# Performance work log

Hardware: AMD Instinct MI355X
Metric: run time of the kernel (lower is better)

## Reference

```python
import jax, jax.numpy as jnp
import numpy as np

MARGIN = 1.0  # init kwarg 'margin'
NUM_CLASSES = 16


def setup_inputs() -> dict:
    key = jax.random.key(0)
    k1, k2 = jax.random.split(key)
    embeddings = jax.random.normal(k1, (384, 1024), dtype=jnp.float32)
    labels = jax.random.randint(k2, (384,), 0, NUM_CLASSES, dtype=jnp.int64)
    return {"embeddings": embeddings, "labels": labels}


def reference(embeddings, labels):
    # Dense, on-device equivalent of the CPU triplet mining:
    # valid triplet (a, p, n) iff labels[a]==labels[p], a<p, labels[n]!=labels[a].
    # Mean over all valid triplets == original torch losses.mean().
    B = embeddings.shape[0]
    sq = jnp.sum(embeddings * embeddings, axis=1)                      # [B]
    # Squared pairwise distances via Gram matrix (same math as (x_i-x_j)^2.sum())
    D = sq[:, None] + sq[None, :] - 2.0 * (embeddings @ embeddings.T)  # [B,B]

    eq = labels[:, None] == labels[None, :]                            # same-label mask [B,B]
    idx = jnp.arange(B)
    ap_valid = eq & (idx[:, None] < idx[None, :])                      # anchor<positive pairs
    mask = ap_valid[:, :, None] & (~eq)[:, None, :]                    # [a,p,n] valid triplets

    # loss[a,p,n] = relu(D[a,p] - D[a,n] + margin)
    loss = jax.nn.relu(D[:, :, None] - D[:, None, :] + MARGIN)         # [B,B,B]

    count = jnp.sum(mask)
    total = jnp.sum(jnp.where(mask, loss, jnp.float32(0.0)))
    mean = jnp.where(count > 0, total / count.astype(loss.dtype), jnp.float32(0.0))
    return mean, count
```

## Files before the change

kernel.cpp:

```cpp
#include <hip/hip_runtime.h>


constexpr int BN  = 384;
constexpr int DIM = 1024;
constexpr float MARGIN = 1.0f;
constexpr int LDK = 68;

__global__ __launch_bounds__(256) void gram_kernel(
    const float* __restrict__ E, float* __restrict__ P,
    float* __restrict__ sqpart, float* __restrict__ total,
    int* __restrict__ cnt, int* __restrict__ ticket, int KC, int NZ) {
    __shared__ float Ast[32 * LDK];
    __shared__ float Bst[32 * LDK];
    const int t    = threadIdx.x;
    const int tile = blockIdx.x % 36;
    const int z    = blockIdx.x / 36;
    const int ti   = tile / 6, tj = tile % 6;
    const int i0   = ti * 64, j0 = tj * 64;

    if (blockIdx.x == 0 && t == 0) { *total = 0.f; *cnt = 0; *ticket = 0; }

    const int r  = t >> 2;
    const int kq = t & 3;
    const int kb = kq * 8;
    const int rs = r ^ (kq << 4);

    const float* Ab = E + (size_t)(i0 + r) * DIM + z * KC + kb;
    const float* Bb = E + (size_t)(j0 + r) * DIM + z * KC + kb;

    float4 a0 = *(const float4*)(Ab);
    float4 a1 = *(const float4*)(Ab + 4);
    float4 b0 = *(const float4*)(Bb);
    float4 b1 = *(const float4*)(Bb + 4);

    const int tx = t & 15, ty = t >> 4;
    float acc[4][4] = {};

    for (int kt = 0; kt < KC; kt += 32) {
        Ast[(kb + 0) * LDK + rs] = a0.x; Ast[(kb + 1) * LDK + rs] = a0.y;
        Ast[(kb + 2) * LDK + rs] = a0.z; Ast[(kb + 3) * LDK + rs] = a0.w;
        Ast[(kb + 4) * LDK + rs] = a1.x; Ast[(kb + 5) * LDK + rs] = a1.y;
        Ast[(kb + 6) * LDK + rs] = a1.z; Ast[(kb + 7) * LDK + rs] = a1.w;
        Bst[(kb + 0) * LDK + rs] = b0.x; Bst[(kb + 1) * LDK + rs] = b0.y;
        Bst[(kb + 2) * LDK + rs] = b0.z; Bst[(kb + 3) * LDK + rs] = b0.w;
        Bst[(kb + 4) * LDK + rs] = b1.x; Bst[(kb + 5) * LDK + rs] = b1.y;
        Bst[(kb + 6) * LDK + rs] = b1.z; Bst[(kb + 7) * LDK + rs] = b1.w;
        __syncthreads();
        if (kt + 32 < KC) {
            a0 = *(const float4*)(Ab + kt + 32);
            a1 = *(const float4*)(Ab + kt + 36);
            b0 = *(const float4*)(Bb + kt + 32);
            b1 = *(const float4*)(Bb + kt + 36);
        }
#pragma unroll
        for (int kk = 0; kk < 32; ++kk) {
            const int sw = (kk >> 3) << 4;
            const float4 av = *(const float4*)&Ast[kk * LDK + ((4 * ty) ^ sw)];
            const float4 bv = *(const float4*)&Bst[kk * LDK + ((4 * tx) ^ sw)];
            const float aa[4] = {av.x, av.y, av.z, av.w};
            const float bb[4] = {bv.x, bv.y, bv.z, bv.w};
#pragma unroll
            for (int i2 = 0; i2 < 4; ++i2)
#pragma unroll
                for (int j2 = 0; j2 < 4; ++j2)
                    acc[i2][j2] += aa[i2] * bb[j2];
        }
        __syncthreads();
    }

    const size_t rowstride = (size_t)NZ * BN;
#pragma unroll
    for (int i2 = 0; i2 < 4; ++i2) {
        *(float4*)&P[(size_t)(i0 + 4 * ty + i2) * rowstride + (size_t)z * BN + (j0 + 4 * tx)] =
            make_float4(acc[i2][0], acc[i2][1], acc[i2][2], acc[i2][3]);
    }
    if (ti == tj && tx == ty) {
#pragma unroll
        for (int i2 = 0; i2 < 4; ++i2)
            sqpart[z * BN + (i0 + 4 * ty + i2)] = acc[i2][i2];
    }
}

template <int NZ>
__global__ __launch_bounds__(128) void triplet_kernel(
    const float* __restrict__ P, const float* __restrict__ sqpart,
    const int* __restrict__ labels, float* __restrict__ total,
    int* __restrict__ cnt, int* __restrict__ ticket, float* __restrict__ out) {
    __shared__ float Hrow[BN];
    __shared__ int   lab[BN];
    __shared__ int   poslist[BN];
    __shared__ int   npos_s;
    __shared__ float wsum[2];
    __shared__ int   wcnt[2];
    const int a   = blockIdx.x;
    const int tid = threadIdx.x;

    if (tid == 0) npos_s = 0;
    for (int i = tid; i < BN; i += 128) lab[i] = labels[i];

    if (tid < 96) {
        const int c0 = tid * 4;
        float4 g = make_float4(0.f, 0.f, 0.f, 0.f);
        float4 s = make_float4(0.f, 0.f, 0.f, 0.f);
#pragma unroll
        for (int z = 0; z < NZ; ++z) {
            const float4 pv = *(const float4*)&P[(size_t)a * ((size_t)NZ * BN) + z * BN + c0];
            const float4 sv = *(const float4*)&sqpart[z * BN + c0];
            g.x += pv.x; g.y += pv.y; g.z += pv.z; g.w += pv.w;
            s.x += sv.x; s.y += sv.y; s.z += sv.z; s.w += sv.w;
        }
        Hrow[c0 + 0] = s.x - 2.f * g.x;
        Hrow[c0 + 1] = s.y - 2.f * g.y;
        Hrow[c0 + 2] = s.z - 2.f * g.z;
        Hrow[c0 + 3] = s.w - 2.f * g.w;
    }
    __syncthreads();

    const int la = lab[a];
    int lc = 0;
#pragma unroll
    for (int q = 0; q < 3; ++q) {
        const int p = tid + q * 128;
        if (lab[p] != la) ++lc;
        else if (p > a) { const int k = atomicAdd(&npos_s, 1); poslist[k] = p; }
    }
    __syncthreads();
    const int np = npos_s;

    const float hn0 = Hrow[tid];
    const float hn1 = Hrow[tid + 128];
    const float hn2 = Hrow[tid + 256];
    const bool  ng0 = (lab[tid]       != la);
    const bool  ng1 = (lab[tid + 128] != la);
    const bool  ng2 = (lab[tid + 256] != la);

    float ls = 0.f;
    for (int k = 0; k < np; ++k) {
        const float dpm = Hrow[poslist[k]] + MARGIN;
        if (ng0) { const float v = dpm - hn0; ls += (v > 0.f) ? v : 0.f; }
        if (ng1) { const float v = dpm - hn1; ls += (v > 0.f) ? v : 0.f; }
        if (ng2) { const float v = dpm - hn2; ls += (v > 0.f) ? v : 0.f; }
    }

#pragma unroll
    for (int off = 32; off; off >>= 1) {
        ls += __shfl_down(ls, off);
        lc += __shfl_down(lc, off);
    }
    const int wave = tid >> 6, lane = tid & 63;
    if (lane == 0) { wsum[wave] = ls; wcnt[wave] = lc; }
    __syncthreads();
    if (tid == 0) {
        const float s    = wsum[0] + wsum[1];
        const int   nneg = wcnt[0] + wcnt[1];
        if (s != 0.f) atomicAdd(total, s);
        if (np)       atomicAdd(cnt, np * nneg);
        __threadfence();
        const int done = atomicAdd(ticket, 1);
        if (done == (int)gridDim.x - 1) {
            const float tot = atomicAdd(total, 0.0f);
            const int   c   = atomicAdd(cnt, 0);
            out[0] = (c > 0) ? tot / (float)c : 0.f;
            out[1] = (float)c;
        }
    }
}

extern "C" void kernel_launch(void* const* d_in, const int* in_sizes, int n_in,
                              void* d_out, int out_size, void* d_ws, size_t ws_size,
                              hipStream_t stream) {
    const float* E      = (const float*)d_in[0];
    const int*   labels = (const int*)d_in[1];
    float*       out    = (float*)d_out;

    int Z = 1;
    for (int cand : {8, 4, 2}) {
        size_t need = (size_t)cand * BN * BN * 4 + (size_t)cand * BN * 4 + 64;
        if (need <= ws_size) { Z = cand; break; }
    }

    char*  ws     = (char*)d_ws;
    float* P      = (float*)ws;
    float* sqpart = (float*)(ws + (size_t)Z * BN * BN * 4);
    float* total  = (float*)(ws + (size_t)Z * BN * BN * 4 + (size_t)Z * BN * 4);
    int*   cnt    = (int*)(total + 1);
    int*   ticket = (int*)(total + 2);

    gram_kernel<<<36 * Z, 256, 0, stream>>>(E, P, sqpart, total, cnt, ticket, DIM / Z, Z);

    switch (Z) {
        case 8:  triplet_kernel<8><<<BN, 128, 0, stream>>>(P, sqpart, labels, total, cnt, ticket, out); break;
        case 4:  triplet_kernel<4><<<BN, 128, 0, stream>>>(P, sqpart, labels, total, cnt, ticket, out); break;
        case 2:  triplet_kernel<2><<<BN, 128, 0, stream>>>(P, sqpart, labels, total, cnt, ticket, out); break;
        default: triplet_kernel<1><<<BN, 128, 0, stream>>>(P, sqpart, labels, total, cnt, ticket, out); break;
    }
}
```

Measured before the change: 83.06 us.

## Split-K into 16 single-stage chunks and widen triplet kernel to one thread per column

The Gram kernel now always splits K into 16 chunks of 64, loading each chunk into shared memory once with no inner K loop. This puts 576 blocks in flight and removes the loop's barriers. The triplet kernel uses 384 threads, one per column. It counts negatives with a per-label shared histogram and precomputes the positive distances plus margin into shared memory, so the inner loop has no branches. The cost is a larger partial-product workspace with no workspace-size check, and a 16-way reduction per element in the triplet stage.

```diff
diff --git a/kernel.cpp b/kernel.cpp
--- a/kernel.cpp
+++ b/kernel.cpp
@@ -1,17 +1,19 @@
 #include <hip/hip_runtime.h>
 
 
-constexpr int BN  = 384;
-constexpr int DIM = 1024;
+constexpr int   BN     = 384;
+constexpr int   DIM    = 1024;
 constexpr float MARGIN = 1.0f;
-constexpr int LDK = 68;
+constexpr int   Z      = 16;
+constexpr int   KC     = DIM / Z;
+constexpr int   LDK    = 68;
 
 __global__ __launch_bounds__(256) void gram_kernel(
     const float* __restrict__ E, float* __restrict__ P,
     float* __restrict__ sqpart, float* __restrict__ total,
-    int* __restrict__ cnt, int* __restrict__ ticket, int KC, int NZ) {
-    __shared__ float Ast[32 * LDK];
-    __shared__ float Bst[32 * LDK];
+    int* __restrict__ cnt, int* __restrict__ ticket) {
+    __shared__ float Ast[KC * LDK];
+    __shared__ float Bst[KC * LDK];
     const int t    = threadIdx.x;
     const int tile = blockIdx.x % 36;
     const int z    = blockIdx.x / 36;
@@ -22,53 +24,44 @@
 
     const int r  = t >> 2;
     const int kq = t & 3;
-    const int kb = kq * 8;
     const int rs = r ^ (kq << 4);
 
-    const float* Ab = E + (size_t)(i0 + r) * DIM + z * KC + kb;
-    const float* Bb = E + (size_t)(j0 + r) * DIM + z * KC + kb;
+    const float* Ab = E + (size_t)(i0 + r) * DIM + z * KC + kq * 16;
+    const float* Bb = E + (size_t)(j0 + r) * DIM + z * KC + kq * 16;
 
-    float4 a0 = *(const float4*)(Ab);
-    float4 a1 = *(const float4*)(Ab + 4);
-    float4 b0 = *(const float4*)(Bb);
-    float4 b1 = *(const float4*)(Bb + 4);
+    float4 a[4], b[4];
+#pragma unroll
+    for (int q = 0; q < 4; ++q) {
+        a[q] = *(const float4*)(Ab + 4 * q);
+        b[q] = *(const float4*)(Bb + 4 * q);
+    }
+#pragma unroll
+    for (int q = 0; q < 4; ++q) {
+        const int kb = kq * 16 + 4 * q;
+        Ast[(kb + 0) * LDK + rs] = a[q].x; Ast[(kb + 1) * LDK + rs] = a[q].y;
+        Ast[(kb + 2) * LDK + rs] = a[q].z; Ast[(kb + 3) * LDK + rs] = a[q].w;
+        Bst[(kb + 0) * LDK + rs] = b[q].x; Bst[(kb + 1) * LDK + rs] = b[q].y;
+        Bst[(kb + 2) * LDK + rs] = b[q].z; Bst[(kb + 3) * LDK + rs] = b[q].w;
+    }
+    __syncthreads();
 
     const int tx = t & 15, ty = t >> 4;
     float acc[4][4] = {};
-
-    for (int kt = 0; kt < KC; kt += 32) {
-        Ast[(kb + 0) * LDK + rs] = a0.x; Ast[(kb + 1) * LDK + rs] = a0.y;
-        Ast[(kb + 2) * LDK + rs] = a0.z; Ast[(kb + 3) * LDK + rs] = a0.w;
-        Ast[(kb + 4) * LDK + rs] = a1.x; Ast[(kb + 5) * LDK + rs] = a1.y;
-        Ast[(kb + 6) * LDK + rs] = a1.z; Ast[(kb + 7) * LDK + rs] = a1.w;
-        Bst[(kb + 0) * LDK + rs] = b0.x; Bst[(kb + 1) * LDK + rs] = b0.y;
-        Bst[(kb + 2) * LDK + rs] = b0.z; Bst[(kb + 3) * LDK + rs] = b0.w;
-        Bst[(kb + 4) * LDK + rs] = b1.x; Bst[(kb + 5) * LDK + rs] = b1.y;
-        Bst[(kb + 6) * LDK + rs] = b1.z; Bst[(kb + 7) * LDK + rs] = b1.w;
-        __syncthreads();
-        if (kt + 32 < KC) {
-            a0 = *(const float4*)(Ab + kt + 32);
-            a1 = *(const float4*)(Ab + kt + 36);
-            b0 = *(const float4*)(Bb + kt + 32);
-            b1 = *(const float4*)(Bb + kt + 36);
-        }
 #pragma unroll
-        for (int kk = 0; kk < 32; ++kk) {
-            const int sw = (kk >> 3) << 4;
-            const float4 av = *(const float4*)&Ast[kk * LDK + ((4 * ty) ^ sw)];
-            const float4 bv = *(const float4*)&Bst[kk * LDK + ((4 * tx) ^ sw)];
-            const float aa[4] = {av.x, av.y, av.z, av.w};
-            const float bb[4] = {bv.x, bv.y, bv.z, bv.w};
+    for (int kk = 0; kk < KC; ++kk) {
+        const int sw = ((kk >> 4) & 3) << 4;
+        const float4 av = *(const float4*)&Ast[kk * LDK + ((4 * ty) ^ sw)];
+        const float4 bv = *(const float4*)&Bst[kk * LDK + ((4 * tx) ^ sw)];
+        const float aa[4] = {av.x, av.y, av.z, av.w};
+        const float bb[4] = {bv.x, bv.y, bv.z, bv.w};
 #pragma unroll
-            for (int i2 = 0; i2 < 4; ++i2)
+        for (int i2 = 0; i2 < 4; ++i2)
 #pragma unroll
-                for (int j2 = 0; j2 < 4; ++j2)
-                    acc[i2][j2] += aa[i2] * bb[j2];
-        }
-        __syncthreads();
+            for (int j2 = 0; j2 < 4; ++j2)
+                acc[i2][j2] = fmaf(aa[i2], bb[j2], acc[i2][j2]);
     }
 
-    const size_t rowstride = (size_t)NZ * BN;
+    const size_t rowstride = (size_t)Z * BN;
 #pragma unroll
     for (int i2 = 0; i2 < 4; ++i2) {
         *(float4*)&P[(size_t)(i0 + 4 * ty + i2) * rowstride + (size_t)z * BN + (j0 + 4 * tx)] =
@@ -82,79 +75,62 @@
 }
 
 template <int NZ>
-__global__ __launch_bounds__(128) void triplet_kernel(
+__global__ __launch_bounds__(BN) void triplet_kernel(
     const float* __restrict__ P, const float* __restrict__ sqpart,
     const int* __restrict__ labels, float* __restrict__ total,
     int* __restrict__ cnt, int* __restrict__ ticket, float* __restrict__ out) {
     __shared__ float Hrow[BN];
-    __shared__ int   lab[BN];
+    __shared__ float Pp[BN];
     __shared__ int   poslist[BN];
     __shared__ int   npos_s;
-    __shared__ float wsum[2];
-    __shared__ int   wcnt[2];
+    __shared__ int   hist[16];
+    __shared__ float wred[BN / 64];
     const int a   = blockIdx.x;
     const int tid = threadIdx.x;
 
-    if (tid == 0) npos_s = 0;
-    for (int i = tid; i < BN; i += 128) lab[i] = labels[i];
-
-    if (tid < 96) {
-        const int c0 = tid * 4;
-        float4 g = make_float4(0.f, 0.f, 0.f, 0.f);
-        float4 s = make_float4(0.f, 0.f, 0.f, 0.f);
-#pragma unroll
-        for (int z = 0; z < NZ; ++z) {
-            const float4 pv = *(const float4*)&P[(size_t)a * ((size_t)NZ * BN) + z * BN + c0];
-            const float4 sv = *(const float4*)&sqpart[z * BN + c0];
-            g.x += pv.x; g.y += pv.y; g.z += pv.z; g.w += pv.w;
-            s.x += sv.x; s.y += sv.y; s.z += sv.z; s.w += sv.w;
-        }
-        Hrow[c0 + 0] = s.x - 2.f * g.x;
-        Hrow[c0 + 1] = s.y - 2.f * g.y;
-        Hrow[c0 + 2] = s.z - 2.f * g.z;
-        Hrow[c0 + 3] = s.w - 2.f * g.w;
-    }
+    if (tid == 0)  npos_s = 0;
+    if (tid < 16)  hist[tid] = 0;
     __syncthreads();
 
-    const int la = lab[a];
-    int lc = 0;
+    const int lj = labels[tid];
+    const int la = labels[a];
+    atomicAdd(&hist[lj], 1);
+    if (lj == la && tid > a) poslist[atomicAdd(&npos_s, 1)] = tid;
+
+    float g = 0.f, s = 0.f;
+    const float* Pa = P + (size_t)a * ((size_t)NZ * BN) + tid;
 #pragma unroll
-    for (int q = 0; q < 3; ++q) {
-        const int p = tid + q * 128;
-        if (lab[p] != la) ++lc;
-        else if (p > a) { const int k = atomicAdd(&npos_s, 1); poslist[k] = p; }
+    for (int zz = 0; zz < NZ; ++zz) {
+        g += Pa[zz * BN];
+        s += sqpart[zz * BN + tid];
     }
+    const float hn = fmaf(-2.f, g, s);
+    Hrow[tid] = hn;
     __syncthreads();
+
     const int np = npos_s;
-
-    const float hn0 = Hrow[tid];
-    const float hn1 = Hrow[tid + 128];
-    const float hn2 = Hrow[tid + 256];
-    const bool  ng0 = (lab[tid]       != la);
-    const bool  ng1 = (lab[tid + 128] != la);
-    const bool  ng2 = (lab[tid + 256] != la);
+    if (tid < np) Pp[tid] = Hrow[poslist[tid]] + MARGIN;
+    __syncthreads();
 
     float ls = 0.f;
-    for (int k = 0; k < np; ++k) {
-        const float dpm = Hrow[poslist[k]] + MARGIN;
-        if (ng0) { const float v = dpm - hn0; ls += (v > 0.f) ? v : 0.f; }
-        if (ng1) { const float v = dpm - hn1; ls += (v > 0.f) ? v : 0.f; }
-        if (ng2) { const float v = dpm - hn2; ls += (v > 0.f) ? v : 0.f; }
+    if (lj != la) {
+        for (int k = 0; k < np; ++k) {
+            const float v = Pp[k] - hn;
+            ls += (v > 0.f) ? v : 0.f;
+        }
     }
 
 #pragma unroll
-    for (int off = 32; off; off >>= 1) {
-        ls += __shfl_down(ls, off);
-        lc += __shfl_down(lc, off);
-    }
-    const int wave = tid >> 6, lane = tid & 63;
-    if (lane == 0) { wsum[wave] = ls; wcnt[wave] = lc; }
+    for (int off = 32; off; off >>= 1) ls += __shfl_down(ls, off);
+    if ((tid & 63) == 0) wred[tid >> 6] = ls;
     __syncthreads();
     if (tid == 0) {
-        const float s    = wsum[0] + wsum[1];
-        const int   nneg = wcnt[0] + wcnt[1];
-        if (s != 0.f) atomicAdd(total, s);
-        if (np)       atomicAdd(cnt, np * nneg);
+        float sum = 0.f;
+#pragma unroll
+        for (int w = 0; w < BN / 64; ++w) sum += wred[w];
+        const int nneg = BN - hist[la];
+        if (sum != 0.f) atomicAdd(total, sum);
+        if (np)         atomicAdd(cnt, np * nneg);
         __threadfence();
         const int done = atomicAdd(ticket, 1);
         if (done == (int)gridDim.x - 1) {
@@ -173,25 +149,13 @@
     const int*   labels = (const int*)d_in[1];
     float*       out    = (float*)d_out;
 
-    int Z = 1;
-    for (int cand : {8, 4, 2}) {
-        size_t need = (size_t)cand * BN * BN * 4 + (size_t)cand * BN * 4 + 64;
-        if (need <= ws_size) { Z = cand; break; }
-    }
-
     char*  ws     = (char*)d_ws;
     float* P      = (float*)ws;
-    float* sqpart = (float*)(ws + (size_t)Z * BN * BN * 4);
-    float* total  = (float*)(ws + (size_t)Z * BN * BN * 4 + (size_t)Z * BN * 4);
+    float* sqpart = (float*)(ws + (size_t)BN * Z * BN * 4);
+    float* total  = (float*)(ws + (size_t)BN * Z * BN * 4 + (size_t)Z * BN * 4);
     int*   cnt    = (int*)(total + 1);
     int*   ticket = (int*)(total + 2);
 
-    gram_kernel<<<36 * Z, 256, 0, stream>>>(E, P, sqpart, total, cnt, ticket, DIM / Z, Z);
-
-    switch (Z) {
-        case 8:  triplet_kernel<8><<<BN, 128, 0, stream>>>(P, sqpart, labels, total, cnt, ticket, out); break;
-        case 4:  triplet_kernel<4><<<BN, 128, 0, stream>>>(P, sqpart, labels, total, cnt, ticket, out); break;
-        case 2:  triplet_kernel<2><<<BN, 128, 0, stream>>>(P, sqpart, labels, total, cnt, ticket, out); break;
-        default: triplet_kernel<1><<<BN, 128, 0, stream>>>(P, sqpart, labels, total, cnt, ticket, out); break;
-    }
+    gram_kernel<<<36 * Z, 256, 0, stream>>>(E, P, sqpart, total, cnt, ticket);
+    triplet_kernel<Z><<<BN, BN, 0, stream>>>(P, sqpart, labels, total, cnt, ticket, out);
 }
```

Measured after the change: 82.80 us. No clear change (-0.3%).
